# Optimization experiments

Measured on AMD Instinct MI355X. Metric: run time of the kernel, lower is better.

## Reference

```python
import jax, jax.numpy as jnp
import numpy as np

N_NODES = 1_000_000
N_EDGES = 32_000_000

def setup_inputs() -> dict:
    key = jax.random.key(0)
    ks = jax.random.split(key, 10)
    s = lambda fan_in: 1.0 / np.sqrt(fan_in)
    return {
        "node_features": jax.random.normal(ks[0], (N_NODES, 2), dtype=jnp.float32),
        "edge_index": jax.random.randint(ks[1], (2, N_EDGES), 0, N_NODES, dtype=jnp.int64) if jax.config.jax_enable_x64 else jax.random.randint(ks[1], (2, N_EDGES), 0, N_NODES, dtype=jnp.int32),
        "W_msg": jax.random.normal(ks[2], (16, 2), dtype=jnp.float32) * s(2),
        "b_msg": jax.random.normal(ks[3], (16,), dtype=jnp.float32) * s(2),
        "W_ih": jax.random.normal(ks[4], (48, 16), dtype=jnp.float32) * s(16),
        "W_hh": jax.random.normal(ks[5], (48, 16), dtype=jnp.float32) * s(16),
        "b_ih": jax.random.normal(ks[6], (48,), dtype=jnp.float32) * s(16),
        "b_hh": jax.random.normal(ks[7], (48,), dtype=jnp.float32) * s(16),
        "W_cls": jax.random.normal(ks[8], (2, 16), dtype=jnp.float32) * s(16),
        "b_cls": jax.random.normal(ks[9], (2,), dtype=jnp.float32) * s(16),
    }

def reference(node_features, edge_index, W_msg, b_msg, W_ih, W_hh, b_ih, b_hh, W_cls, b_cls):
    N = node_features.shape[0]
    src, dst = edge_index[0], edge_index[1]
    # segment-mean of predecessor features (predecessors of dst are src)
    sums = jax.ops.segment_sum(node_features[src], dst, num_segments=N)  # [N,2]
    cnt = jax.ops.segment_sum(jnp.ones(src.shape, node_features.dtype), dst, num_segments=N)  # [N]
    has_pred = cnt > 0
    agg = jnp.where(has_pred[:, None], sums / jnp.maximum(cnt, 1.0)[:, None], node_features)
    # msg linear: [N,16]
    x = agg @ W_msg.T + b_msg
    # single-step GRU with h0 = 0 (torch nn.GRU gate math)
    h0 = jnp.zeros_like(x)
    gi = x @ W_ih.T + b_ih   # [N,48]
    gh = h0 @ W_hh.T + b_hh  # [N,48]
    i_r, i_z, i_n = jnp.split(gi, 3, axis=-1)
    h_r, h_z, h_n = jnp.split(gh, 3, axis=-1)
    r = jax.nn.sigmoid(i_r + h_r)
    z = jax.nn.sigmoid(i_z + h_z)
    n = jnp.tanh(i_n + r * h_n)
    h = (1.0 - z) * n + z * h0
    # classifier: [N,2]
    return h @ W_cls.T + b_cls
```

## Files before the change

kernel.cpp:

```cpp
#include <hip/hip_runtime.h>


#define NBKT        256
#define BKT_SHIFT   12
#define DLOW_MASK   4095u
#define BKT_CAP     139264u
#define CHUNK       16384
#define BIN_THREADS 512
#define ACC_THREADS 1024
#define SPLIT       2
#define BKT_RANGE   4096
#define NODE_SPACE  (NBKT * BKT_RANGE)

__device__ __forceinline__ unsigned long long expand_pkt(unsigned p20)
{
    return (1ull << 52) | ((unsigned long long)(p20 >> 10) << 26)
                        | (unsigned long long)(p20 & 1023u);
}

__device__ __forceinline__ unsigned gather_sc0(const unsigned* p)
{
    return __hip_atomic_load(p, __ATOMIC_RELAXED, __HIP_MEMORY_SCOPE_AGENT);
}

__global__ __launch_bounds__(256) void tgnn_prep_kernel(
    const float* __restrict__ W_msg, const float* __restrict__ b_msg,
    const float* __restrict__ W_ih,  const float* __restrict__ b_ih,
    const float* __restrict__ b_hh,  const float* __restrict__ W_cls,
    const float* __restrict__ b_cls, float* __restrict__ P,
    unsigned* __restrict__ cursor)
{
    int j = threadIdx.x;
    cursor[j] = (unsigned)j * BKT_CAP;
    if (j < 48) {
        float a0 = 0.f, a1 = 0.f, dd = 0.f;
        #pragma unroll
        for (int k = 0; k < 16; ++k) {
            float w = W_ih[j * 16 + k];
            a0 += w * W_msg[k * 2 + 0];
            a1 += w * W_msg[k * 2 + 1];
            dd += w * b_msg[k];
        }
        dd += b_ih[j];
        P[j]      = a0;
        P[48 + j] = a1;
        if (j < 16)      P[96 + j]         = dd + b_hh[j];
        else if (j < 32) P[112 + (j - 16)] = dd + b_hh[j];
        else             P[128 + (j - 32)] = dd;
    }
    if (j < 16) {
        P[144 + j] = b_hh[32 + j];
        P[160 + j] = W_cls[j];
        P[176 + j] = W_cls[16 + j];
    }
    if (j == 0) { P[192] = b_cls[0]; P[193] = b_cls[1]; }
}

__global__ __launch_bounds__(256) void tgnn_quant_kernel(
    const float2* __restrict__ nf, unsigned* __restrict__ qnf, int n)
{
    int i = blockIdx.x * blockDim.x + threadIdx.x;
    if (i >= n) return;
    float2 f = nf[i];
    float x = fminf(fmaxf(f.x, -7.9f), 7.9f);
    float y = fminf(fmaxf(f.y, -7.9f), 7.9f);
    unsigned qx = (unsigned)fmaf(x, 64.0f, 512.5f);
    unsigned qy = (unsigned)fmaf(y, 64.0f, 512.5f);
    qnf[i] = qx | (qy << 10);
}

__global__ __launch_bounds__(BIN_THREADS) void tgnn_bin_kernel(
    const int* __restrict__ src, const int* __restrict__ dst,
    const unsigned* __restrict__ qnf,
    unsigned* __restrict__ rec, unsigned* __restrict__ cursor,
    unsigned long long* __restrict__ partial0,
    int n_edges)
{
    __shared__ unsigned cnt[NBKT];
    __shared__ unsigned pos[NBKT];
    __shared__ unsigned scur[NBKT];
    __shared__ unsigned gbase[NBKT];
    __shared__ unsigned stage[CHUNK];

    int t  = threadIdx.x;
    int e0 = blockIdx.x * CHUNK;
    int ne = n_edges - e0;
    if (ne <= 0) return;
    if (ne > CHUNK) ne = CHUNK;
    int nv4 = (ne + 3) >> 2;

    const int4* s4p = (const int4*)(src + e0);
    const int4* d4p = (const int4*)(dst + e0);

    int4 dr[8];
    unsigned q[32];
    #pragma unroll
    for (int j = 0; j < 8; ++j) {
        int i4 = j * BIN_THREADS + t;
        if (i4 < nv4) {
            dr[j] = d4p[i4];
            int4 s = s4p[i4];
            q[4 * j + 0] = gather_sc0(qnf + (unsigned)s.x);
            q[4 * j + 1] = gather_sc0(qnf + (unsigned)s.y);
            q[4 * j + 2] = gather_sc0(qnf + (unsigned)s.z);
            q[4 * j + 3] = gather_sc0(qnf + (unsigned)s.w);
        } else {
            dr[j] = make_int4(0, 0, 0, 0);
            q[4 * j + 0] = q[4 * j + 1] = q[4 * j + 2] = q[4 * j + 3] = 0;
        }
    }

    if (t < NBKT) cnt[t] = 0;
    __syncthreads();

    #pragma unroll
    for (int j = 0; j < 8; ++j) {
        int base = 4 * (j * BIN_THREADS + t);
        if (base < ne) {
            int lim = ne - base;
            int dv[4] = { dr[j].x, dr[j].y, dr[j].z, dr[j].w };
            #pragma unroll
            for (int c = 0; c < 4; ++c)
                if (c < lim) atomicAdd(&cnt[((unsigned)dv[c]) >> BKT_SHIFT], 1u);
        }
    }
    __syncthreads();

    if (t < NBKT) pos[t] = cnt[t];
    __syncthreads();
    #pragma unroll
    for (int off = 1; off < NBKT; off <<= 1) {
        unsigned v = 0, a = 0;
        if (t < NBKT) { v = pos[t]; a = (t >= off) ? pos[t - off] : 0u; }
        __syncthreads();
        if (t < NBKT) pos[t] = v + a;
        __syncthreads();
    }
    if (t < NBKT) {
        unsigned myCnt  = cnt[t];
        unsigned myBase = pos[t] - myCnt;
        scur[t] = myBase;
        pos[t]  = myBase;
        gbase[t] = myCnt ? atomicAdd(&cursor[t], myCnt) : 0u;
    }
    __syncthreads();

    #pragma unroll
    for (int j = 0; j < 8; ++j) {
        int base = 4 * (j * BIN_THREADS + t);
        if (base < ne) {
            int lim = ne - base;
            int dv[4] = { dr[j].x, dr[j].y, dr[j].z, dr[j].w };
            #pragma unroll
            for (int c = 0; c < 4; ++c) if (c < lim) {
                unsigned d = (unsigned)dv[c];
                unsigned b = d >> BKT_SHIFT;
                unsigned p = atomicAdd(&scur[b], 1u);
                stage[p] = (q[4 * j + c] << 12) | (d & DLOW_MASK);
            }
        }
    }
    __syncthreads();

    int wave = t >> 6, lane = t & 63;
    for (int b = wave; b < NBKT; b += BIN_THREADS / 64) {
        unsigned n = cnt[b];
        if (!n) continue;
        unsigned sb = pos[b];
        unsigned gb = gbase[b];
        unsigned capEnd = (unsigned)(b + 1) * BKT_CAP;
        for (unsigned i = lane; i < n; i += 64) {
            unsigned r = stage[sb + i];
            unsigned slot = gb + i;
            if (slot < capEnd) {
                rec[slot] = r;
            } else {
                unsigned node = ((unsigned)b << BKT_SHIFT) | (r & DLOW_MASK);
                atomicAdd(&partial0[node], expand_pkt(r >> 12));
            }
        }
    }
}

__global__ __launch_bounds__(ACC_THREADS) void tgnn_accum_kernel(
    const unsigned* __restrict__ rec,
    const unsigned* __restrict__ cursor,
    unsigned long long* __restrict__ partial)
{
    __shared__ unsigned long long acc[BKT_RANGE];
    int b = blockIdx.x >> 1;
    int s = blockIdx.x & 1;
    int t = threadIdx.x;

    unsigned count = cursor[b] - (unsigned)b * BKT_CAP;
    if (count > BKT_CAP) count = BKT_CAP;
    unsigned mid = (count >> 1) & ~3u;
    unsigned i0 = s ? mid : 0u;
    unsigned i1 = s ? count : mid;

    unsigned long long* pb = partial + (size_t)s * NODE_SPACE + (size_t)b * BKT_RANGE;
    if (s == 0) {
        #pragma unroll
        for (int k = 0; k < BKT_RANGE / ACC_THREADS; ++k)
            acc[k * ACC_THREADS + t] = pb[k * ACC_THREADS + t];
    } else {
        #pragma unroll
        for (int k = 0; k < BKT_RANGE / ACC_THREADS; ++k)
            acc[k * ACC_THREADS + t] = 0ull;
    }
    __syncthreads();

    const unsigned* rb  = rec + (size_t)b * BKT_CAP;
    const int4*     rb4 = (const int4*)rb;

    unsigned v0 = i0 >> 2;
    unsigned v1 = i1 >> 2;
    for (unsigned v = v0 + t; v < v1; v += ACC_THREADS) {
        int4 ra = rb4[v];
        unsigned r0 = (unsigned)ra.x, r1 = (unsigned)ra.y;
        unsigned r2 = (unsigned)ra.z, r3 = (unsigned)ra.w;
        atomicAdd(&acc[r0 & DLOW_MASK], expand_pkt(r0 >> 12));
        atomicAdd(&acc[r1 & DLOW_MASK], expand_pkt(r1 >> 12));
        atomicAdd(&acc[r2 & DLOW_MASK], expand_pkt(r2 >> 12));
        atomicAdd(&acc[r3 & DLOW_MASK], expand_pkt(r3 >> 12));
    }
    for (unsigned i = (v1 << 2) + t; i < i1; i += ACC_THREADS) {
        unsigned r = rb[i];
        atomicAdd(&acc[r & DLOW_MASK], expand_pkt(r >> 12));
    }
    __syncthreads();

    #pragma unroll
    for (int k = 0; k < BKT_RANGE / ACC_THREADS; ++k)
        pb[k * ACC_THREADS + t] = acc[k * ACC_THREADS + t];
}

__global__ __launch_bounds__(256) void tgnn_merge_node_kernel(
    const float2* __restrict__ nf,
    const unsigned long long* __restrict__ partial,
    const float* __restrict__ P,
    float2* __restrict__ out, int n_nodes)
{
    __shared__ float p[194];
    for (int k = threadIdx.x; k < 194; k += 256) p[k] = P[k];
    __syncthreads();

    int i = blockIdx.x * 256 + threadIdx.x;
    if (i >= n_nodes) return;

    unsigned long long v = partial[i] + partial[NODE_SPACE + i];
    unsigned c = (unsigned)(v >> 52);
    float a0, a1;
    if (c > 0) {
        float inv = 1.0f / (float)c;
        float X = (float)(unsigned)(v & 0x3FFFFFFull);
        float Y = (float)(unsigned)((v >> 26) & 0x3FFFFFFull);
        a0 = X * inv * (1.0f / 64.0f) - 8.0f;
        a1 = Y * inv * (1.0f / 64.0f) - 8.0f;
    } else {
        float2 f = nf[i];
        a0 = f.x;
        a1 = f.y;
    }

    float o0 = p[192], o1 = p[193];
    #pragma unroll
    for (int j = 0; j < 16; ++j) {
        float gr = fmaf(p[j],      a0, fmaf(p[48 + j], a1, p[96 + j]));
        float gz = fmaf(p[16 + j], a0, fmaf(p[64 + j], a1, p[112 + j]));
        float gn = fmaf(p[32 + j], a0, fmaf(p[80 + j], a1, p[128 + j]));
        float r  = 1.0f / (1.0f + __expf(-gr));
        float z  = 1.0f / (1.0f + __expf(-gz));
        float tt = fmaf(r, p[144 + j], gn);
        tt = fminf(fmaxf(tt, -12.0f), 12.0f);
        float e  = __expf(2.0f * tt);
        float n  = (e - 1.0f) / (e + 1.0f);
        float h  = (1.0f - z) * n;
        o0 = fmaf(p[160 + j], h, o0);
        o1 = fmaf(p[176 + j], h, o1);
    }
    out[i] = make_float2(o0, o1);
}

__global__ __launch_bounds__(256) void tgnn_edge_kernel(
    const unsigned* __restrict__ qnf,
    const int* __restrict__ src,
    const int* __restrict__ dst,
    unsigned long long* __restrict__ pack,
    int n_edges)
{
    int tid    = blockIdx.x * blockDim.x + threadIdx.x;
    int stride = gridDim.x * blockDim.x;
    int n4     = n_edges >> 2;
    const int4* __restrict__ src4 = (const int4*)src;
    const int4* __restrict__ dst4 = (const int4*)dst;
    for (int i = tid; i < n4; i += stride) {
        int4 s = src4[i];
        int4 d = dst4[i];
        unsigned q0 = qnf[s.x], q1 = qnf[s.y], q2 = qnf[s.z], q3 = qnf[s.w];
        atomicAdd(&pack[d.x], expand_pkt(q0));
        atomicAdd(&pack[d.y], expand_pkt(q1));
        atomicAdd(&pack[d.z], expand_pkt(q2));
        atomicAdd(&pack[d.w], expand_pkt(q3));
    }
    for (int e = (n4 << 2) + tid; e < n_edges; e += stride)
        atomicAdd(&pack[dst[e]], expand_pkt(qnf[src[e]]));
}

__global__ __launch_bounds__(256) void tgnn_node_kernel(
    const float2* __restrict__ nf,
    const unsigned long long* __restrict__ pack,
    const float* __restrict__ P,
    float2* __restrict__ out, int n_nodes)
{
    __shared__ float p[194];
    for (int k = threadIdx.x; k < 194; k += 256) p[k] = P[k];
    __syncthreads();
    int i = blockIdx.x * 256 + threadIdx.x;
    if (i >= n_nodes) return;
    unsigned long long v = pack[i];
    unsigned c = (unsigned)(v >> 52);
    float a0, a1;
    if (c > 0) {
        float inv = 1.0f / (float)c;
        float X = (float)(unsigned)(v & 0x3FFFFFFull);
        float Y = (float)(unsigned)((v >> 26) & 0x3FFFFFFull);
        a0 = X * inv * (1.0f / 64.0f) - 8.0f;
        a1 = Y * inv * (1.0f / 64.0f) - 8.0f;
    } else {
        float2 f = nf[i];
        a0 = f.x; a1 = f.y;
    }
    float o0 = p[192], o1 = p[193];
    #pragma unroll
    for (int j = 0; j < 16; ++j) {
        float gr = fmaf(p[j],      a0, fmaf(p[48 + j], a1, p[96 + j]));
        float gz = fmaf(p[16 + j], a0, fmaf(p[64 + j], a1, p[112 + j]));
        float gn = fmaf(p[32 + j], a0, fmaf(p[80 + j], a1, p[128 + j]));
        float r  = 1.0f / (1.0f + __expf(-gr));
        float z  = 1.0f / (1.0f + __expf(-gz));
        float tt = fmaf(r, p[144 + j], gn);
        tt = fminf(fmaxf(tt, -12.0f), 12.0f);
        float e  = __expf(2.0f * tt);
        float n  = (e - 1.0f) / (e + 1.0f);
        float h  = (1.0f - z) * n;
        o0 = fmaf(p[160 + j], h, o0);
        o1 = fmaf(p[176 + j], h, o1);
    }
    out[i] = make_float2(o0, o1);
}

extern "C" void kernel_launch(void* const* d_in, const int* in_sizes, int n_in,
                              void* d_out, int out_size, void* d_ws, size_t ws_size,
                              hipStream_t stream)
{
    const float* nf    = (const float*)d_in[0];
    const int*   ei    = (const int*)d_in[1];
    const float* W_msg = (const float*)d_in[2];
    const float* b_msg = (const float*)d_in[3];
    const float* W_ih  = (const float*)d_in[4];
    const float* b_ih  = (const float*)d_in[6];
    const float* b_hh  = (const float*)d_in[7];
    const float* W_cls = (const float*)d_in[8];
    const float* b_cls = (const float*)d_in[9];
    float* out = (float*)d_out;

    const int N = in_sizes[0] / 2;
    const int E = in_sizes[1] / 2;
    const int qBlocks = (N + 255) / 256;

    size_t off = 0;
    auto take = [&](size_t bytes) { size_t o = off; off = (off + bytes + 255) & ~(size_t)255; return o; };
    size_t partialOff = take((size_t)SPLIT * NODE_SPACE * 8);
    size_t recOff     = take((size_t)NBKT * BKT_CAP * 4);
    size_t qnfOff     = take((size_t)N * 4);
    size_t curOff     = take((size_t)NBKT * 4);
    size_t pOff       = take(194 * 4);
    size_t need = off;

    char* ws = (char*)d_ws;

    if (ws_size >= need) {
        unsigned long long* partial = (unsigned long long*)(ws + partialOff);
        unsigned* rec    = (unsigned*)(ws + recOff);
        unsigned* qnf    = (unsigned*)(ws + qnfOff);
        unsigned* cursor = (unsigned*)(ws + curOff);
        float*    P      = (float*)(ws + pOff);

        (void)hipMemsetAsync(partial, 0, (size_t)NODE_SPACE * 8, stream);

        tgnn_prep_kernel<<<1, 256, 0, stream>>>(W_msg, b_msg, W_ih, b_ih, b_hh,
                                                W_cls, b_cls, P, cursor);
        tgnn_quant_kernel<<<qBlocks, 256, 0, stream>>>((const float2*)nf, qnf, N);

        int binBlocks = (E + CHUNK - 1) / CHUNK;
        tgnn_bin_kernel<<<binBlocks, BIN_THREADS, 0, stream>>>(ei, ei + E, qnf, rec,
                                                               cursor, partial, E);

        tgnn_accum_kernel<<<NBKT * SPLIT, ACC_THREADS, 0, stream>>>(rec, cursor,
                                                                    partial);

        tgnn_merge_node_kernel<<<qBlocks, 256, 0, stream>>>((const float2*)nf, partial,
                                                            P, (float2*)out, N);
    } else {
        unsigned long long* pack = (unsigned long long*)ws;
        unsigned* qnf = (unsigned*)(ws + (size_t)N * 8);
        float*    P   = (float*)(ws + (size_t)N * 12);
        unsigned* cursorDummy = (unsigned*)(ws + (size_t)N * 12 + 1024);

        (void)hipMemsetAsync(pack, 0, (size_t)N * 8, stream);
        tgnn_prep_kernel<<<1, 256, 0, stream>>>(W_msg, b_msg, W_ih, b_ih, b_hh,
                                                W_cls, b_cls, P, cursorDummy);
        tgnn_quant_kernel<<<qBlocks, 256, 0, stream>>>((const float2*)nf, qnf, N);
        tgnn_edge_kernel<<<2048, 256, 0, stream>>>(qnf, ei, ei + E, pack, E);
        tgnn_node_kernel<<<qBlocks, 256, 0, stream>>>((const float2*)nf, pack,
                                                      P, (float2*)out, N);
    }
}
```

Measured before the change: 334.0 us.

## Replace random source gather with two-pass radix binning by source then destination

```diff
diff --git a/kernel.cpp b/kernel.cpp
--- a/kernel.cpp
+++ b/kernel.cpp
@@ -7,6 +7,8 @@
 #define BKT_CAP     139264u
 #define CHUNK       16384
 #define BIN_THREADS 512
+#define CHUNK2      8192
+#define SLICES2     ((BKT_CAP + CHUNK2 - 1) / CHUNK2)
 #define ACC_THREADS 1024
 #define SPLIT       2
 #define BKT_RANGE   4096
@@ -16,11 +18,6 @@
 {
     return (1ull << 52) | ((unsigned long long)(p20 >> 10) << 26)
                         | (unsigned long long)(p20 & 1023u);
-}
-
-__device__ __forceinline__ unsigned gather_sc0(const unsigned* p)
-{
-    return __hip_atomic_load(p, __ATOMIC_RELAXED, __HIP_MEMORY_SCOPE_AGENT);
 }
 
 __global__ __launch_bounds__(256) void tgnn_prep_kernel(
@@ -28,10 +25,11 @@
     const float* __restrict__ W_ih,  const float* __restrict__ b_ih,
     const float* __restrict__ b_hh,  const float* __restrict__ W_cls,
     const float* __restrict__ b_cls, float* __restrict__ P,
-    unsigned* __restrict__ cursor)
+    unsigned* __restrict__ cursor1, unsigned* __restrict__ cursor2)
 {
     int j = threadIdx.x;
-    cursor[j] = (unsigned)j * BKT_CAP;
+    cursor1[j] = (unsigned)j * BKT_CAP;
+    cursor2[j] = (unsigned)j * BKT_CAP;
     if (j < 48) {
         float a0 = 0.f, a1 = 0.f, dd = 0.f;
         #pragma unroll
@@ -69,10 +67,10 @@
     qnf[i] = qx | (qy << 10);
 }
 
-__global__ __launch_bounds__(BIN_THREADS) void tgnn_bin_kernel(
+__global__ __launch_bounds__(BIN_THREADS) void tgnn_bin1_kernel(
     const int* __restrict__ src, const int* __restrict__ dst,
     const unsigned* __restrict__ qnf,
-    unsigned* __restrict__ rec, unsigned* __restrict__ cursor,
+    unsigned* __restrict__ rec1, unsigned* __restrict__ cursor1,
     unsigned long long* __restrict__ partial0,
     int n_edges)
 {
@@ -92,22 +90,12 @@
     const int4* s4p = (const int4*)(src + e0);
     const int4* d4p = (const int4*)(dst + e0);
 
-    int4 dr[8];
-    unsigned q[32];
+    int4 dr[8], sr[8];
     #pragma unroll
     for (int j = 0; j < 8; ++j) {
         int i4 = j * BIN_THREADS + t;
-        if (i4 < nv4) {
-            dr[j] = d4p[i4];
-            int4 s = s4p[i4];
-            q[4 * j + 0] = gather_sc0(qnf + (unsigned)s.x);
-            q[4 * j + 1] = gather_sc0(qnf + (unsigned)s.y);
-            q[4 * j + 2] = gather_sc0(qnf + (unsigned)s.z);
-            q[4 * j + 3] = gather_sc0(qnf + (unsigned)s.w);
-        } else {
-            dr[j] = make_int4(0, 0, 0, 0);
-            q[4 * j + 0] = q[4 * j + 1] = q[4 * j + 2] = q[4 * j + 3] = 0;
-        }
+        if (i4 < nv4) { dr[j] = d4p[i4]; sr[j] = s4p[i4]; }
+        else { dr[j] = make_int4(0,0,0,0); sr[j] = make_int4(0,0,0,0); }
     }
 
     if (t < NBKT) cnt[t] = 0;
@@ -118,10 +106,10 @@
         int base = 4 * (j * BIN_THREADS + t);
         if (base < ne) {
             int lim = ne - base;
-            int dv[4] = { dr[j].x, dr[j].y, dr[j].z, dr[j].w };
+            int sv[4] = { sr[j].x, sr[j].y, sr[j].z, sr[j].w };
             #pragma unroll
             for (int c = 0; c < 4; ++c)
-                if (c < lim) atomicAdd(&cnt[((unsigned)dv[c]) >> BKT_SHIFT], 1u);
+                if (c < lim) atomicAdd(&cnt[((unsigned)sv[c]) >> BKT_SHIFT], 1u);
         }
     }
     __syncthreads();
@@ -141,7 +129,7 @@
         unsigned myBase = pos[t] - myCnt;
         scur[t] = myBase;
         pos[t]  = myBase;
-        gbase[t] = myCnt ? atomicAdd(&cursor[t], myCnt) : 0u;
+        gbase[t] = myCnt ? atomicAdd(&cursor1[t], myCnt) : 0u;
     }
     __syncthreads();
 
@@ -150,13 +138,14 @@
         int base = 4 * (j * BIN_THREADS + t);
         if (base < ne) {
             int lim = ne - base;
+            int sv[4] = { sr[j].x, sr[j].y, sr[j].z, sr[j].w };
             int dv[4] = { dr[j].x, dr[j].y, dr[j].z, dr[j].w };
             #pragma unroll
             for (int c = 0; c < 4; ++c) if (c < lim) {
-                unsigned d = (unsigned)dv[c];
-                unsigned b = d >> BKT_SHIFT;
+                unsigned s = (unsigned)sv[c];
+                unsigned b = s >> BKT_SHIFT;
                 unsigned p = atomicAdd(&scur[b], 1u);
-                stage[p] = (q[4 * j + c] << 12) | (d & DLOW_MASK);
+                stage[p] = ((unsigned)dv[c] << 12) | (s & DLOW_MASK);
             }
         }
     }
@@ -173,9 +162,121 @@
             unsigned r = stage[sb + i];
             unsigned slot = gb + i;
             if (slot < capEnd) {
-                rec[slot] = r;
+                rec1[slot] = r;
             } else {
-                unsigned node = ((unsigned)b << BKT_SHIFT) | (r & DLOW_MASK);
+                unsigned node = r >> 12;
+                unsigned s    = ((unsigned)b << BKT_SHIFT) | (r & DLOW_MASK);
+                atomicAdd(&partial0[node], expand_pkt(qnf[s]));
+            }
+        }
+    }
+}
+
+__global__ __launch_bounds__(256) void tgnn_pass2_kernel(
+    const unsigned* __restrict__ rec1, const unsigned* __restrict__ cursor1,
+    const unsigned* __restrict__ qnf,
+    unsigned* __restrict__ rec2, unsigned* __restrict__ cursor2,
+    unsigned long long* __restrict__ partial0)
+{
+    __shared__ unsigned qlds[BKT_RANGE];
+    __shared__ unsigned cnt[NBKT];
+    __shared__ unsigned pos[NBKT];
+    __shared__ unsigned scur[NBKT];
+    __shared__ unsigned gbase[NBKT];
+    __shared__ unsigned stage[CHUNK2];
+
+    int b = blockIdx.y;
+    int t = threadIdx.x;
+
+    unsigned count = cursor1[b] - (unsigned)b * BKT_CAP;
+    if (count > BKT_CAP) count = BKT_CAP;
+    unsigned i0 = (unsigned)blockIdx.x * CHUNK2;
+    if (i0 >= count) return;
+    unsigned ne = count - i0;
+    if (ne > CHUNK2) ne = CHUNK2;
+    int nv4 = (int)((ne + 3) >> 2);
+
+    const unsigned* qsrc = qnf + (size_t)b * BKT_RANGE;
+    #pragma unroll
+    for (int k = 0; k < BKT_RANGE / 256; ++k)
+        qlds[k * 256 + t] = qsrc[k * 256 + t];
+
+    const int4* r4p = (const int4*)(rec1 + (size_t)b * BKT_CAP + i0);
+    int4 rr[8];
+    #pragma unroll
+    for (int j = 0; j < 8; ++j) {
+        int i4 = j * 256 + t;
+        rr[j] = (i4 < nv4) ? r4p[i4] : make_int4(0, 0, 0, 0);
+    }
+
+    cnt[t] = 0;
+    __syncthreads();
+
+    #pragma unroll
+    for (int j = 0; j < 8; ++j) {
+        int base = 4 * (j * 256 + t);
+        if (base < (int)ne) {
+            int lim = (int)ne - base;
+            unsigned rv[4] = { (unsigned)rr[j].x, (unsigned)rr[j].y,
+                               (unsigned)rr[j].z, (unsigned)rr[j].w };
+            #pragma unroll
+            for (int c = 0; c < 4; ++c)
+                if (c < lim) atomicAdd(&cnt[rv[c] >> 24], 1u);
+        }
+    }
+    __syncthreads();
+
+    pos[t] = cnt[t];
+    __syncthreads();
+    #pragma unroll
+    for (int off = 1; off < NBKT; off <<= 1) {
+        unsigned v = pos[t];
+        unsigned a = (t >= off) ? pos[t - off] : 0u;
+        __syncthreads();
+        pos[t] = v + a;
+        __syncthreads();
+    }
+    {
+        unsigned myCnt  = cnt[t];
+        unsigned myBase = pos[t] - myCnt;
+        scur[t] = myBase;
+        pos[t]  = myBase;
+        gbase[t] = myCnt ? atomicAdd(&cursor2[t], myCnt) : 0u;
+    }
+    __syncthreads();
+
+    #pragma unroll
+    for (int j = 0; j < 8; ++j) {
+        int base = 4 * (j * 256 + t);
+        if (base < (int)ne) {
+            int lim = (int)ne - base;
+            unsigned rv[4] = { (unsigned)rr[j].x, (unsigned)rr[j].y,
+                               (unsigned)rr[j].z, (unsigned)rr[j].w };
+            #pragma unroll
+            for (int c = 0; c < 4; ++c) if (c < lim) {
+                unsigned r  = rv[c];
+                unsigned bb = r >> 24;
+                unsigned p  = atomicAdd(&scur[bb], 1u);
+                stage[p] = (qlds[r & DLOW_MASK] << 12) | ((r >> 12) & DLOW_MASK);
+            }
+        }
+    }
+    __syncthreads();
+
+    int wave = t >> 6, lane = t & 63;
+    for (int bb = wave; bb < NBKT; bb += 4) {
+        unsigned n = cnt[bb];
+        if (!n) continue;
+        unsigned sb = pos[bb];
+        unsigned gb = gbase[bb];
+        unsigned capEnd = (unsigned)(bb + 1) * BKT_CAP;
+        for (unsigned i = lane; i < n; i += 64) {
+            unsigned r = stage[sb + i];
+            unsigned slot = gb + i;
+            if (slot < capEnd) {
+                rec2[slot] = r;
+            } else {
+                unsigned node = ((unsigned)bb << BKT_SHIFT) | (r & DLOW_MASK);
                 atomicAdd(&partial0[node], expand_pkt(r >> 12));
             }
         }
@@ -183,8 +284,8 @@
 }
 
 __global__ __launch_bounds__(ACC_THREADS) void tgnn_accum_kernel(
-    const unsigned* __restrict__ rec,
-    const unsigned* __restrict__ cursor,
+    const unsigned* __restrict__ rec2,
+    const unsigned* __restrict__ cursor2,
     unsigned long long* __restrict__ partial)
 {
     __shared__ unsigned long long acc[BKT_RANGE];
@@ -192,7 +293,7 @@
     int s = blockIdx.x & 1;
     int t = threadIdx.x;
 
-    unsigned count = cursor[b] - (unsigned)b * BKT_CAP;
+    unsigned count = cursor2[b] - (unsigned)b * BKT_CAP;
     if (count > BKT_CAP) count = BKT_CAP;
     unsigned mid = (count >> 1) & ~3u;
     unsigned i0 = s ? mid : 0u;
@@ -210,7 +311,7 @@
     }
     __syncthreads();
 
-    const unsigned* rb  = rec + (size_t)b * BKT_CAP;
+    const unsigned* rb  = rec2 + (size_t)b * BKT_CAP;
     const int4*     rb4 = (const int4*)rb;
 
     unsigned v0 = i0 >> 2;
@@ -372,9 +473,11 @@
     size_t off = 0;
     auto take = [&](size_t bytes) { size_t o = off; off = (off + bytes + 255) & ~(size_t)255; return o; };
     size_t partialOff = take((size_t)SPLIT * NODE_SPACE * 8);
-    size_t recOff     = take((size_t)NBKT * BKT_CAP * 4);
+    size_t rec1Off    = take((size_t)NBKT * BKT_CAP * 4);
+    size_t rec2Off    = take((size_t)NBKT * BKT_CAP * 4);
     size_t qnfOff     = take((size_t)N * 4);
-    size_t curOff     = take((size_t)NBKT * 4);
+    size_t cur1Off    = take((size_t)NBKT * 4);
+    size_t cur2Off    = take((size_t)NBKT * 4);
     size_t pOff       = take(194 * 4);
     size_t need = off;
 
@@ -382,22 +485,29 @@
 
     if (ws_size >= need) {
         unsigned long long* partial = (unsigned long long*)(ws + partialOff);
-        unsigned* rec    = (unsigned*)(ws + recOff);
-        unsigned* qnf    = (unsigned*)(ws + qnfOff);
-        unsigned* cursor = (unsigned*)(ws + curOff);
-        float*    P      = (float*)(ws + pOff);
+        unsigned* rec1    = (unsigned*)(ws + rec1Off);
+        unsigned* rec2    = (unsigned*)(ws + rec2Off);
+        unsigned* qnf     = (unsigned*)(ws + qnfOff);
+        unsigned* cursor1 = (unsigned*)(ws + cur1Off);
+        unsigned* cursor2 = (unsigned*)(ws + cur2Off);
+        float*    P       = (float*)(ws + pOff);
 
         (void)hipMemsetAsync(partial, 0, (size_t)NODE_SPACE * 8, stream);
 
         tgnn_prep_kernel<<<1, 256, 0, stream>>>(W_msg, b_msg, W_ih, b_ih, b_hh,
-                                                W_cls, b_cls, P, cursor);
+                                                W_cls, b_cls, P, cursor1, cursor2);
         tgnn_quant_kernel<<<qBlocks, 256, 0, stream>>>((const float2*)nf, qnf, N);
 
         int binBlocks = (E + CHUNK - 1) / CHUNK;
-        tgnn_bin_kernel<<<binBlocks, BIN_THREADS, 0, stream>>>(ei, ei + E, qnf, rec,
-                                                               cursor, partial, E);
-
-        tgnn_accum_kernel<<<NBKT * SPLIT, ACC_THREADS, 0, stream>>>(rec, cursor,
+        tgnn_bin1_kernel<<<binBlocks, BIN_THREADS, 0, stream>>>(ei, ei + E, qnf,
+                                                                rec1, cursor1,
+                                                                partial, E);
+
+        dim3 g2(SLICES2, NBKT);
+        tgnn_pass2_kernel<<<g2, 256, 0, stream>>>(rec1, cursor1, qnf,
+                                                  rec2, cursor2, partial);
+
+        tgnn_accum_kernel<<<NBKT * SPLIT, ACC_THREADS, 0, stream>>>(rec2, cursor2,
                                                                     partial);
 
         tgnn_merge_node_kernel<<<qBlocks, 256, 0, stream>>>((const float2*)nf, partial,
@@ -406,11 +516,12 @@
         unsigned long long* pack = (unsigned long long*)ws;
         unsigned* qnf = (unsigned*)(ws + (size_t)N * 8);
         float*    P   = (float*)(ws + (size_t)N * 12);
-        unsigned* cursorDummy = (unsigned*)(ws + (size_t)N * 12 + 1024);
+        unsigned* curD1 = (unsigned*)(ws + (size_t)N * 12 + 1024);
+        unsigned* curD2 = (unsigned*)(ws + (size_t)N * 12 + 3072);
 
         (void)hipMemsetAsync(pack, 0, (size_t)N * 8, stream);
         tgnn_prep_kernel<<<1, 256, 0, stream>>>(W_msg, b_msg, W_ih, b_ih, b_hh,
-                                                W_cls, b_cls, P, cursorDummy);
+                                                W_cls, b_cls, P, curD1, curD2);
         tgnn_quant_kernel<<<qBlocks, 256, 0, stream>>>((const float2*)nf, qnf, N);
         tgnn_edge_kernel<<<2048, 256, 0, stream>>>(qnf, ei, ei + E, pack, E);
         tgnn_node_kernel<<<qBlocks, 256, 0, stream>>>((const float2*)nf, pack,
```

New measurement: 325.2 us. 1.03x faster.
